# Optimization experiments

Measured on AMD Instinct MI355X. Metric: run time of the kernel, lower is better.

The kernel has to match this reference:

```python
import jax, jax.numpy as jnp
import numpy as np

EPS = 0.1          # sinkhorn_epsilon
N_ITER = 100       # sinkhorn_max_iter (fixed-iteration log-domain Sinkhorn)


def setup_inputs() -> dict:
    key = jax.random.key(0)
    k1, k2 = jax.random.split(key)
    B, S, D = 16, 1024, 2048
    student_outputs = jax.random.normal(k1, (B, S, D), dtype=jnp.float32)
    teacher_outputs = jax.random.normal(k2, (B, S, D), dtype=jnp.float32)
    return {"student_outputs": student_outputs, "teacher_outputs": teacher_outputs}


def _cosine_cost(x1, x2):
    # x1: [B, n1, D] (teacher), x2: [B, n2, D] (student)
    x1n = x1 / jnp.linalg.norm(x1, axis=-1, keepdims=True).clip(1e-12)
    x2n = x2 / jnp.linalg.norm(x2, axis=-1, keepdims=True).clip(1e-12)
    cos = jnp.einsum('bnd,bmd->bnm', x1n, x2n)
    return 1.0 - (cos + 1.0) / 2.0  # [B, n1, n2]


def _sinkhorn_log(C, loga, logb):
    # Log-domain (stabilized) Sinkhorn; C: [n1, n2]
    def body(carry, _):
        f, g = carry
        f = EPS * (loga - jax.nn.logsumexp((g[None, :] - C) / EPS, axis=1))
        g = EPS * (logb - jax.nn.logsumexp((f[:, None] - C) / EPS, axis=0))
        return (f, g), None
    f0 = jnp.zeros_like(loga)
    g0 = jnp.zeros_like(logb)
    (f, g), _ = jax.lax.scan(body, (f0, g0), None, length=N_ITER)
    return jnp.exp((f[:, None] + g[None, :] - C) / EPS)  # transport plan P


def reference(student_outputs, teacher_outputs):
    B, n1, _ = teacher_outputs.shape
    n2 = student_outputs.shape[1]
    C = _cosine_cost(teacher_outputs, student_outputs)  # [B, n1, n2]
    loga = jnp.full((n1,), -jnp.log(jnp.float32(n1)), dtype=C.dtype)  # uniform weights
    logb = jnp.full((n2,), -jnp.log(jnp.float32(n2)), dtype=C.dtype)
    P = jax.vmap(lambda c: _sinkhorn_log(c, loga, logb))(C)  # [B, n1, n2]
    # In the original, P is computed in numpy (detached); only C carries grads.
    P = jax.lax.stop_gradient(P)
    return jnp.sum(P * C, axis=(1, 2)).mean()
```

## Files before the change

### kernel.cpp

```cpp
#include <hip/hip_runtime.h>
#include <math.h>

#define BATCH 16
#define SEQ   1024
#define DIM   2048
#define EPS_F 0.1f
#define INV_EPS 10.0f
#define N_ITER 100

typedef short bf16x8 __attribute__((ext_vector_type(8)));
typedef float f32x4  __attribute__((ext_vector_type(4)));

__device__ inline float blo(unsigned int x) { return __uint_as_float(x << 16); }
__device__ inline float bhi(unsigned int x) { return __uint_as_float(x & 0xffff0000u); }

__device__ inline unsigned short f_to_bf16(float f) {
    unsigned int x = __float_as_uint(f);
    unsigned int lsb = (x >> 16) & 1u;
    x += 0x7fffu + lsb;
    return (unsigned short)(x >> 16);
}

__global__ void init_state(float* __restrict__ tbuf, unsigned int* __restrict__ flags) {
    int i = blockIdx.x * 256 + threadIdx.x;
    ((float4*)tbuf)[i] = (float4){0.f, 0.f, 0.f, 0.f};
    if (i < 1024) flags[i] = 0u;
}

__global__ __launch_bounds__(256) void normalize_kernel(
    const float* __restrict__ student, const float* __restrict__ teacher,
    unsigned short* __restrict__ Sn, unsigned short* __restrict__ Tn)
{
    int rowid  = blockIdx.x;
    int tensor = rowid >> 14;
    int row    = rowid & 16383;
    const float* src = tensor ? teacher : student;
    unsigned short* dst = tensor ? Tn : Sn;
    const float4* p4 = (const float4*)(src + (size_t)row * DIM);
    int t = threadIdx.x;

    float4 a = p4[t];
    float4 b = p4[t + 256];
    float ss = a.x*a.x + a.y*a.y + a.z*a.z + a.w*a.w
             + b.x*b.x + b.y*b.y + b.z*b.z + b.w*b.w;
    #pragma unroll
    for (int m = 32; m; m >>= 1) ss += __shfl_xor(ss, m, 64);
    __shared__ float wss[4];
    if ((t & 63) == 0) wss[t >> 6] = ss;
    __syncthreads();
    float rn = 1.0f / fmaxf(sqrtf(wss[0] + wss[1] + wss[2] + wss[3]), 1e-12f);

    unsigned short o1[4], o2[4];
    o1[0] = f_to_bf16(a.x * rn); o1[1] = f_to_bf16(a.y * rn);
    o1[2] = f_to_bf16(a.z * rn); o1[3] = f_to_bf16(a.w * rn);
    o2[0] = f_to_bf16(b.x * rn); o2[1] = f_to_bf16(b.y * rn);
    o2[2] = f_to_bf16(b.z * rn); o2[3] = f_to_bf16(b.w * rn);
    unsigned short* d = dst + (size_t)row * DIM;
    *(uint2*)(d + 4*t)        = *(uint2*)o1;
    *(uint2*)(d + 1024 + 4*t) = *(uint2*)o2;
}

#define TM  128
#define BK  32
#define LDK 40

__global__ __launch_bounds__(256) void gemm_cost_kernel(
    const unsigned short* __restrict__ Tn, const unsigned short* __restrict__ Sn,
    unsigned short* __restrict__ Kmat)
{
    __shared__ unsigned short As[TM * LDK];
    __shared__ unsigned short Bs[TM * LDK];

    int bid  = blockIdx.x;
    int b    = bid >> 6;
    int tile = bid & 63;
    int tm0  = (tile >> 3) * TM;
    int tn0  = (tile & 7)  * TM;

    const unsigned short* Ab = Tn + (size_t)b * SEQ * DIM;
    const unsigned short* Bb = Sn + (size_t)b * SEQ * DIM;

    int t    = threadIdx.x;
    int w    = t >> 6;
    int l    = t & 63;
    int mq   = (w >> 1) * 64;
    int nq   = (w & 1)  * 64;
    int lrow = l & 15;
    int kg   = l >> 4;

    int srow = t >> 2;
    int sseg = t & 3;

    f32x4 acc[4][4];
    #pragma unroll
    for (int i = 0; i < 4; i++)
        #pragma unroll
        for (int j = 0; j < 4; j++)
            acc[i][j] = (f32x4){0.f, 0.f, 0.f, 0.f};

    for (int k0 = 0; k0 < DIM; k0 += BK) {
        const int4 va0 = *(const int4*)(Ab + (size_t)(tm0 + srow)      * DIM + k0 + sseg * 8);
        const int4 va1 = *(const int4*)(Ab + (size_t)(tm0 + srow + 64) * DIM + k0 + sseg * 8);
        const int4 vb0 = *(const int4*)(Bb + (size_t)(tn0 + srow)      * DIM + k0 + sseg * 8);
        const int4 vb1 = *(const int4*)(Bb + (size_t)(tn0 + srow + 64) * DIM + k0 + sseg * 8);
        __syncthreads();
        *(int4*)&As[(srow)      * LDK + sseg * 8] = va0;
        *(int4*)&As[(srow + 64) * LDK + sseg * 8] = va1;
        *(int4*)&Bs[(srow)      * LDK + sseg * 8] = vb0;
        *(int4*)&Bs[(srow + 64) * LDK + sseg * 8] = vb1;
        __syncthreads();

        bf16x8 af[4], bfr[4];
        #pragma unroll
        for (int i = 0; i < 4; i++)
            af[i] = *(const bf16x8*)&As[(mq + i * 16 + lrow) * LDK + kg * 8];
        #pragma unroll
        for (int j = 0; j < 4; j++)
            bfr[j] = *(const bf16x8*)&Bs[(nq + j * 16 + lrow) * LDK + kg * 8];
        #pragma unroll
        for (int i = 0; i < 4; i++)
            #pragma unroll
            for (int j = 0; j < 4; j++)
                acc[i][j] = __builtin_amdgcn_mfma_f32_16x16x32_bf16(af[i], bfr[j], acc[i][j], 0, 0, 0);
    }

    unsigned short* Kb = Kmat + ((size_t)b << 20);
    #pragma unroll
    for (int i = 0; i < 4; i++) {
        #pragma unroll
        for (int j = 0; j < 4; j++) {
            int gcol = tn0 + nq + j * 16 + lrow;
            #pragma unroll
            for (int r = 0; r < 4; r++) {
                int grow = tm0 + mq + i * 16 + kg * 4 + r;
                float cosv = acc[i][j][r];
                float cost = 0.5f - 0.5f * cosv;
                Kb[((size_t)grow << 10) + gcol] = f_to_bf16(__expf(-cost * INV_EPS));
            }
        }
    }
}

__global__ __launch_bounds__(512) void sinkhorn_persistent(
    const unsigned short* __restrict__ Kmat,
    float* __restrict__ tbuf,
    unsigned int* __restrict__ flags,
    float* __restrict__ partials)
{
    __shared__ float part[8 * 1024];
    __shared__ float vsw[1024];
    __shared__ float ulds[64];
    __shared__ float wlds[8];

    int idx   = blockIdx.x;
    int b     = (idx & 7) | (((idx >> 3) & 1) << 3);
    int slice = idx >> 4;
    const unsigned short* Kb = Kmat + ((size_t)b << 20);
    float* tb = tbuf + (b << 12);
    unsigned int* flag = flags + b * 64;

    int t    = threadIdx.x;
    int lane = t & 63;
    int w    = t >> 6;
    int r0   = slice << 6;

    vsw[t] = 1.0f; vsw[t + 512] = 1.0f;
    __syncthreads();

    unsigned int tgt = 0;
    for (int iter = 0; iter < N_ITER; iter++) {
        float vreg[16];
        #pragma unroll
        for (int k = 0; k < 16; k++) vreg[k] = vsw[k * 64 + lane];

        float tacc[16];
        #pragma unroll
        for (int k = 0; k < 16; k++) tacc[k] = 0.f;

        #pragma unroll
        for (int rr = 0; rr < 8; rr++) {
            int row = r0 + w * 8 + rr;
            const unsigned int* kp = (const unsigned int*)(Kb + ((size_t)row << 10) + (lane << 4));
            unsigned int k0 = kp[0], k1 = kp[1], k2 = kp[2], k3 = kp[3];
            unsigned int k4 = kp[4], k5 = kp[5], k6 = kp[6], k7 = kp[7];
            float f0  = blo(k0), f1  = bhi(k0), f2  = blo(k1), f3  = bhi(k1);
            float f4  = blo(k2), f5  = bhi(k2), f6  = blo(k3), f7  = bhi(k3);
            float f8  = blo(k4), f9  = bhi(k4), f10 = blo(k5), f11 = bhi(k5);
            float f12 = blo(k6), f13 = bhi(k6), f14 = blo(k7), f15 = bhi(k7);
            float s = 0.f;
            s = fmaf(f0,  vreg[0],  s); s = fmaf(f1,  vreg[1],  s);
            s = fmaf(f2,  vreg[2],  s); s = fmaf(f3,  vreg[3],  s);
            s = fmaf(f4,  vreg[4],  s); s = fmaf(f5,  vreg[5],  s);
            s = fmaf(f6,  vreg[6],  s); s = fmaf(f7,  vreg[7],  s);
            s = fmaf(f8,  vreg[8],  s); s = fmaf(f9,  vreg[9],  s);
            s = fmaf(f10, vreg[10], s); s = fmaf(f11, vreg[11], s);
            s = fmaf(f12, vreg[12], s); s = fmaf(f13, vreg[13], s);
            s = fmaf(f14, vreg[14], s); s = fmaf(f15, vreg[15], s);
            #pragma unroll
            for (int m = 32; m; m >>= 1) s += __shfl_xor(s, m, 64);
            float ui = (1.0f / 1024.0f) / s;
            if (lane == 0) ulds[w * 8 + rr] = ui;
            tacc[0]  = fmaf(f0,  ui, tacc[0]);  tacc[1]  = fmaf(f1,  ui, tacc[1]);
            tacc[2]  = fmaf(f2,  ui, tacc[2]);  tacc[3]  = fmaf(f3,  ui, tacc[3]);
            tacc[4]  = fmaf(f4,  ui, tacc[4]);  tacc[5]  = fmaf(f5,  ui, tacc[5]);
            tacc[6]  = fmaf(f6,  ui, tacc[6]);  tacc[7]  = fmaf(f7,  ui, tacc[7]);
            tacc[8]  = fmaf(f8,  ui, tacc[8]);  tacc[9]  = fmaf(f9,  ui, tacc[9]);
            tacc[10] = fmaf(f10, ui, tacc[10]); tacc[11] = fmaf(f11, ui, tacc[11]);
            tacc[12] = fmaf(f12, ui, tacc[12]); tacc[13] = fmaf(f13, ui, tacc[13]);
            tacc[14] = fmaf(f14, ui, tacc[14]); tacc[15] = fmaf(f15, ui, tacc[15]);
        }
        #pragma unroll
        for (int k = 0; k < 16; k += 4)
            *(float4*)&part[w * 1024 + lane * 16 + k] =
                (float4){tacc[k], tacc[k+1], tacc[k+2], tacc[k+3]};
        __syncthreads();

        float a0 = 0.f, a1 = 0.f;
        #pragma unroll
        for (int g = 0; g < 8; g++) {
            float2 p = *(const float2*)&part[g * 1024 + t * 2];
            a0 += p.x; a1 += p.y;
        }
        int cur = iter & 3;
        float* tcur = tb + (cur << 10);
        atomicAdd(&tcur[t * 2],     a0);
        atomicAdd(&tcur[t * 2 + 1], a1);
        if (t < 64)
            __hip_atomic_store(&tb[(((iter + 2) & 3) << 10) + r0 + t], 0.0f,
                               __ATOMIC_RELAXED, __HIP_MEMORY_SCOPE_AGENT);
        __syncthreads();

        tgt += 16;
        if (t == 0) {
            __hip_atomic_fetch_add(flag, 1u, __ATOMIC_RELAXED, __HIP_MEMORY_SCOPE_AGENT);
            while (__hip_atomic_load(flag, __ATOMIC_RELAXED, __HIP_MEMORY_SCOPE_AGENT) < tgt)
                __builtin_amdgcn_s_sleep(2);
        }
        __syncthreads();

        float t0 = __hip_atomic_load(&tcur[t * 2],     __ATOMIC_RELAXED, __HIP_MEMORY_SCOPE_AGENT);
        float t1 = __hip_atomic_load(&tcur[t * 2 + 1], __ATOMIC_RELAXED, __HIP_MEMORY_SCOPE_AGENT);
        int c0 = t * 2, c1 = t * 2 + 1;
        vsw[(c0 & 15) * 64 + (c0 >> 4)] = (1.0f / 1024.0f) / t0;
        vsw[(c1 & 15) * 64 + (c1 >> 4)] = (1.0f / 1024.0f) / t1;
        __syncthreads();
    }

    {
        float vreg[16];
        #pragma unroll
        for (int k = 0; k < 16; k++) vreg[k] = vsw[k * 64 + lane];
        float wsum = 0.f;
        #pragma unroll
        for (int rr = 0; rr < 8; rr++) {
            int row = r0 + w * 8 + rr;
            const unsigned int* kp = (const unsigned int*)(Kb + ((size_t)row << 10) + (lane << 4));
            float s = 0.f;
            #pragma unroll
            for (int q = 0; q < 8; q++) {
                unsigned int kk = kp[q];
                float klo = blo(kk), khi = bhi(kk);
                float clo = -EPS_F * __logf(klo);
                float chi = -EPS_F * __logf(khi);
                s = fmaf(klo * vreg[2 * q],     clo, s);
                s = fmaf(khi * vreg[2 * q + 1], chi, s);
            }
            #pragma unroll
            for (int m = 32; m; m >>= 1) s += __shfl_xor(s, m, 64);
            if (lane == 0) wsum += s * ulds[w * 8 + rr];
        }
        if (lane == 0) wlds[w] = wsum;
    }
    __syncthreads();
    if (t == 0) {
        float s = 0.f;
        #pragma unroll
        for (int g = 0; g < 8; g++) s += wlds[g];
        partials[idx] = s;
    }
}

__global__ __launch_bounds__(256) void loss_final(
    const float* __restrict__ partials, float* __restrict__ out)
{
    int t = threadIdx.x;
    float s = partials[t];
    #pragma unroll
    for (int m = 32; m; m >>= 1) s += __shfl_xor(s, m, 64);
    __shared__ float wp[4];
    if ((t & 63) == 0) wp[t >> 6] = s;
    __syncthreads();
    if (t == 0) out[0] = (wp[0] + wp[1] + wp[2] + wp[3]) * (1.0f / 16.0f);
}

extern "C" void kernel_launch(void* const* d_in, const int* in_sizes, int n_in,
                              void* d_out, int out_size, void* d_ws, size_t ws_size,
                              hipStream_t stream) {
    const float* student = (const float*)d_in[0];
    const float* teacher = (const float*)d_in[1];
    float* out = (float*)d_out;
    char* ws = (char*)d_ws;

    unsigned short* Tn   = (unsigned short*)(ws);
    unsigned short* Sn   = (unsigned short*)(ws + 67108864);
    unsigned short* Kmat = (unsigned short*)(ws + 134217728);
    float*        tbuf     = (float*)(ws + 167772160);
    unsigned int* flags    = (unsigned int*)(ws + 167772160 + 262144);
    float*        partials = (float*)(ws + 167772160 + 266240);

    hipLaunchKernelGGL(init_state, dim3(64), dim3(256), 0, stream, tbuf, flags);
    hipLaunchKernelGGL(normalize_kernel, dim3(32768), dim3(256), 0, stream,
                       student, teacher, Sn, Tn);
    hipLaunchKernelGGL(gemm_cost_kernel, dim3(1024), dim3(256), 0, stream, Tn, Sn, Kmat);
    hipLaunchKernelGGL(sinkhorn_persistent, dim3(256), dim3(512), 0, stream,
                       Kmat, tbuf, flags, partials);
    hipLaunchKernelGGL(loss_final, dim3(1), dim3(256), 0, stream, partials, out);
}
```

Before: 875.4 us.

## Cache each block's K slice in LDS and batch row reductions in Sinkhorn loop

```diff
diff --git a/kernel.cpp b/kernel.cpp
--- a/kernel.cpp
+++ b/kernel.cpp
@@ -141,14 +141,21 @@
     }
 }
 
-__global__ __launch_bounds__(512) void sinkhorn_persistent(
+#define UNPK(A,B,F) do { \
+    F[0]=blo(A.x);  F[1]=bhi(A.x);  F[2]=blo(A.y);  F[3]=bhi(A.y);  \
+    F[4]=blo(A.z);  F[5]=bhi(A.z);  F[6]=blo(A.w);  F[7]=bhi(A.w);  \
+    F[8]=blo(B.x);  F[9]=bhi(B.x);  F[10]=blo(B.y); F[11]=bhi(B.y); \
+    F[12]=blo(B.z); F[13]=bhi(B.z); F[14]=blo(B.w); F[15]=bhi(B.w); } while(0)
+
+__global__ __launch_bounds__(512, 2) void sinkhorn_persistent(
     const unsigned short* __restrict__ Kmat,
     float* __restrict__ tbuf,
     unsigned int* __restrict__ flags,
     float* __restrict__ partials)
 {
-    __shared__ float part[8 * 1024];
+    __shared__ __align__(16) unsigned short Ks[64 * 1024];
     __shared__ float vsw[1024];
+    __shared__ float part[1024];
     __shared__ float ulds[64];
     __shared__ float wlds[8];
 
@@ -164,67 +171,92 @@
     int w    = t >> 6;
     int r0   = slice << 6;
 
+    int sw   = (lane >> 2) & 1;
+    int sw8  = sw << 3;
+    int xa   = (lane << 5) ^ (sw << 4);
+    int xb   = xa ^ 16;
+    int phx  = ((lane >> 1) & 1) << 2;
+    const char* ksb = (const char*)Ks;
+
+    {
+        const int4* src = (const int4*)(Kb + ((size_t)r0 << 10));
+        int4* dst = (int4*)Ks;
+        #pragma unroll
+        for (int i = 0; i < 16; i++) dst[t + i * 512] = src[t + i * 512];
+    }
     vsw[t] = 1.0f; vsw[t + 512] = 1.0f;
+    part[t] = 0.f; part[t + 512] = 0.f;
     __syncthreads();
 
     unsigned int tgt = 0;
     for (int iter = 0; iter < N_ITER; iter++) {
         float vreg[16];
         #pragma unroll
-        for (int k = 0; k < 16; k++) vreg[k] = vsw[k * 64 + lane];
+        for (int k = 0; k < 16; k++) vreg[k] = vsw[((k ^ sw8) << 6) + lane];
 
         float tacc[16];
         #pragma unroll
         for (int k = 0; k < 16; k++) tacc[k] = 0.f;
 
         #pragma unroll
-        for (int rr = 0; rr < 8; rr++) {
-            int row = r0 + w * 8 + rr;
-            const unsigned int* kp = (const unsigned int*)(Kb + ((size_t)row << 10) + (lane << 4));
-            unsigned int k0 = kp[0], k1 = kp[1], k2 = kp[2], k3 = kp[3];
-            unsigned int k4 = kp[4], k5 = kp[5], k6 = kp[6], k7 = kp[7];
-            float f0  = blo(k0), f1  = bhi(k0), f2  = blo(k1), f3  = bhi(k1);
-            float f4  = blo(k2), f5  = bhi(k2), f6  = blo(k3), f7  = bhi(k3);
-            float f8  = blo(k4), f9  = bhi(k4), f10 = blo(k5), f11 = bhi(k5);
-            float f12 = blo(k6), f13 = bhi(k6), f14 = blo(k7), f15 = bhi(k7);
-            float s = 0.f;
-            s = fmaf(f0,  vreg[0],  s); s = fmaf(f1,  vreg[1],  s);
-            s = fmaf(f2,  vreg[2],  s); s = fmaf(f3,  vreg[3],  s);
-            s = fmaf(f4,  vreg[4],  s); s = fmaf(f5,  vreg[5],  s);
-            s = fmaf(f6,  vreg[6],  s); s = fmaf(f7,  vreg[7],  s);
-            s = fmaf(f8,  vreg[8],  s); s = fmaf(f9,  vreg[9],  s);
-            s = fmaf(f10, vreg[10], s); s = fmaf(f11, vreg[11], s);
-            s = fmaf(f12, vreg[12], s); s = fmaf(f13, vreg[13], s);
-            s = fmaf(f14, vreg[14], s); s = fmaf(f15, vreg[15], s);
-            #pragma unroll
-            for (int m = 32; m; m >>= 1) s += __shfl_xor(s, m, 64);
-            float ui = (1.0f / 1024.0f) / s;
-            if (lane == 0) ulds[w * 8 + rr] = ui;
-            tacc[0]  = fmaf(f0,  ui, tacc[0]);  tacc[1]  = fmaf(f1,  ui, tacc[1]);
-            tacc[2]  = fmaf(f2,  ui, tacc[2]);  tacc[3]  = fmaf(f3,  ui, tacc[3]);
-            tacc[4]  = fmaf(f4,  ui, tacc[4]);  tacc[5]  = fmaf(f5,  ui, tacc[5]);
-            tacc[6]  = fmaf(f6,  ui, tacc[6]);  tacc[7]  = fmaf(f7,  ui, tacc[7]);
-            tacc[8]  = fmaf(f8,  ui, tacc[8]);  tacc[9]  = fmaf(f9,  ui, tacc[9]);
-            tacc[10] = fmaf(f10, ui, tacc[10]); tacc[11] = fmaf(f11, ui, tacc[11]);
-            tacc[12] = fmaf(f12, ui, tacc[12]); tacc[13] = fmaf(f13, ui, tacc[13]);
-            tacc[14] = fmaf(f14, ui, tacc[14]); tacc[15] = fmaf(f15, ui, tacc[15]);
+        for (int bb = 0; bb < 2; bb++) {
+            const char* kr = ksb + (((w << 3) + (bb << 2)) << 11);
+            uint4 a0 = *(const uint4*)(kr + xa);
+            uint4 b0 = *(const uint4*)(kr + xb);
+            uint4 a1 = *(const uint4*)(kr + 2048 + xa);
+            uint4 b1 = *(const uint4*)(kr + 2048 + xb);
+            uint4 a2 = *(const uint4*)(kr + 4096 + xa);
+            uint4 b2 = *(const uint4*)(kr + 4096 + xb);
+            uint4 a3 = *(const uint4*)(kr + 6144 + xa);
+            uint4 b3 = *(const uint4*)(kr + 6144 + xb);
+            float f0[16], f1[16], f2[16], f3[16];
+            UNPK(a0, b0, f0); UNPK(a1, b1, f1);
+            UNPK(a2, b2, f2); UNPK(a3, b3, f3);
+
+            float s0 = 0.f, s1 = 0.f, s2 = 0.f, s3 = 0.f;
+            #pragma unroll
+            for (int k = 0; k < 16; k++) {
+                s0 = fmaf(f0[k], vreg[k], s0);
+                s1 = fmaf(f1[k], vreg[k], s1);
+                s2 = fmaf(f2[k], vreg[k], s2);
+                s3 = fmaf(f3[k], vreg[k], s3);
+            }
+            #pragma unroll
+            for (int m = 32; m; m >>= 1) {
+                s0 += __shfl_xor(s0, m, 64);
+                s1 += __shfl_xor(s1, m, 64);
+                s2 += __shfl_xor(s2, m, 64);
+                s3 += __shfl_xor(s3, m, 64);
+            }
+            float u0 = (1.0f / 1024.0f) / s0;
+            float u1 = (1.0f / 1024.0f) / s1;
+            float u2 = (1.0f / 1024.0f) / s2;
+            float u3 = (1.0f / 1024.0f) / s3;
+            if (lane == 0) {
+                int rb = (w << 3) + (bb << 2);
+                ulds[rb] = u0; ulds[rb + 1] = u1; ulds[rb + 2] = u2; ulds[rb + 3] = u3;
+            }
+            #pragma unroll
+            for (int k = 0; k < 16; k++) {
+                tacc[k] = fmaf(f0[k], u0, tacc[k]);
+                tacc[k] = fmaf(f1[k], u1, tacc[k]);
+                tacc[k] = fmaf(f2[k], u2, tacc[k]);
+                tacc[k] = fmaf(f3[k], u3, tacc[k]);
+            }
         }
         #pragma unroll
-        for (int k = 0; k < 16; k += 4)
-            *(float4*)&part[w * 1024 + lane * 16 + k] =
-                (float4){tacc[k], tacc[k+1], tacc[k+2], tacc[k+3]};
-        __syncthreads();
-
-        float a0 = 0.f, a1 = 0.f;
-        #pragma unroll
-        for (int g = 0; g < 8; g++) {
-            float2 p = *(const float2*)&part[g * 1024 + t * 2];
-            a0 += p.x; a1 += p.y;
-        }
+        for (int k = 0; k < 16; k++)
+            atomicAdd(&part[((lane << 4) + (k ^ sw8)) ^ phx], tacc[k]);
+        __syncthreads();
+
         int cur = iter & 3;
         float* tcur = tb + (cur << 10);
-        atomicAdd(&tcur[t * 2],     a0);
-        atomicAdd(&tcur[t * 2 + 1], a1);
+        int c0 = t * 2;
+        int p0 = c0 ^ (((c0 >> 5) & 1) << 2);
+        float2 pv = *(const float2*)&part[p0];
+        atomicAdd(&tcur[c0],     pv.x);
+        atomicAdd(&tcur[c0 + 1], pv.y);
+        *(float2*)&part[p0] = (float2){0.f, 0.f};
         if (t < 64)
             __hip_atomic_store(&tb[(((iter + 2) & 3) << 10) + r0 + t], 0.0f,
                                __ATOMIC_RELAXED, __HIP_MEMORY_SCOPE_AGENT);
@@ -238,36 +270,34 @@
         }
         __syncthreads();
 
-        float t0 = __hip_atomic_load(&tcur[t * 2],     __ATOMIC_RELAXED, __HIP_MEMORY_SCOPE_AGENT);
-        float t1 = __hip_atomic_load(&tcur[t * 2 + 1], __ATOMIC_RELAXED, __HIP_MEMORY_SCOPE_AGENT);
-        int c0 = t * 2, c1 = t * 2 + 1;
-        vsw[(c0 & 15) * 64 + (c0 >> 4)] = (1.0f / 1024.0f) / t0;
-        vsw[(c1 & 15) * 64 + (c1 >> 4)] = (1.0f / 1024.0f) / t1;
+        float t0 = __hip_atomic_load(&tcur[c0],     __ATOMIC_RELAXED, __HIP_MEMORY_SCOPE_AGENT);
+        float t1 = __hip_atomic_load(&tcur[c0 + 1], __ATOMIC_RELAXED, __HIP_MEMORY_SCOPE_AGENT);
+        int c1 = c0 + 1;
+        vsw[((c0 & 15) << 6) + (c0 >> 4)] = (1.0f / 1024.0f) / t0;
+        vsw[((c1 & 15) << 6) + (c1 >> 4)] = (1.0f / 1024.0f) / t1;
         __syncthreads();
     }
 
     {
         float vreg[16];
         #pragma unroll
-        for (int k = 0; k < 16; k++) vreg[k] = vsw[k * 64 + lane];
+        for (int k = 0; k < 16; k++) vreg[k] = vsw[((k ^ sw8) << 6) + lane];
         float wsum = 0.f;
         #pragma unroll
         for (int rr = 0; rr < 8; rr++) {
-            int row = r0 + w * 8 + rr;
-            const unsigned int* kp = (const unsigned int*)(Kb + ((size_t)row << 10) + (lane << 4));
+            const char* kr = ksb + (((w << 3) + rr) << 11);
+            uint4 A = *(const uint4*)(kr + xa);
+            uint4 B = *(const uint4*)(kr + xb);
+            float f[16]; UNPK(A, B, f);
             float s = 0.f;
             #pragma unroll
-            for (int q = 0; q < 8; q++) {
-                unsigned int kk = kp[q];
-                float klo = blo(kk), khi = bhi(kk);
-                float clo = -EPS_F * __logf(klo);
-                float chi = -EPS_F * __logf(khi);
-                s = fmaf(klo * vreg[2 * q],     clo, s);
-                s = fmaf(khi * vreg[2 * q + 1], chi, s);
+            for (int k = 0; k < 16; k++) {
+                float c = -EPS_F * __logf(f[k]);
+                s = fmaf(f[k] * vreg[k], c, s);
             }
             #pragma unroll
             for (int m = 32; m; m >>= 1) s += __shfl_xor(s, m, 64);
-            if (lane == 0) wsum += s * ulds[w * 8 + rr];
+            if (lane == 0) wsum += s * ulds[(w << 3) + rr];
         }
         if (lane == 0) wlds[w] = wsum;
     }
```

New measurement: 1.847 ms. 2.11x slower.
